# Performance work log

Measured on AMD Instinct MI355X. Metric: run time of the kernel, lower is better.

Reference implementation:

```python
import jax, jax.numpy as jnp
import numpy as np

FEAT = 128
N_RBF = 20
CUTOFF = 5.0
N_GRAPHS = 128
ATOMS = 64
N_ATOMS = N_GRAPHS * ATOMS  # 8192
N_EDGES = N_ATOMS * 32      # 262144


def setup_inputs() -> dict:
    key = jax.random.key(0)
    ks = jax.random.split(key, 12)
    s_j = jax.random.normal(ks[0], (N_ATOMS, FEAT), jnp.float32)
    v_j = jax.random.normal(ks[1], (N_ATOMS, FEAT, 3), jnp.float32)
    r_ij = jax.random.normal(ks[2], (N_EDGES, 3), jnp.float32) * 1.5
    nbrs = jax.random.randint(ks[3], (N_EDGES, 2), 0, N_ATOMS, dtype=jnp.int32)
    num_atoms = jnp.full((N_GRAPHS,), ATOMS, dtype=jnp.int32)
    sc = 0.05
    W1 = jax.random.normal(ks[4], (FEAT, FEAT), jnp.float32) * sc
    b1 = jnp.zeros((FEAT,), jnp.float32)
    W2 = jax.random.normal(ks[5], (FEAT, 3 * FEAT), jnp.float32) * sc
    b2 = jnp.zeros((3 * FEAT,), jnp.float32)
    Wr = jax.random.normal(ks[6], (N_RBF, 3 * FEAT), jnp.float32) * sc
    br = jnp.zeros((3 * FEAT,), jnp.float32)
    Wd = jax.random.normal(ks[7], (FEAT, 3 * FEAT), jnp.float32) * sc
    bd = jnp.zeros((3 * FEAT,), jnp.float32)
    return {"s_j": s_j, "v_j": v_j, "r_ij": r_ij, "nbrs": nbrs,
            "num_atoms": num_atoms, "W1": W1, "b1": b1, "W2": W2, "b2": b2,
            "Wr": Wr, "br": br, "Wd": Wd, "bd": bd}


def _forward(s_j, v_j, r_ij, nbrs, W1, b1, W2, b2, Wr, br, Wd, bd):
    # preprocess_r
    dist = jnp.linalg.norm(r_ij, axis=-1)            # [E]
    unit = r_ij / dist[:, None]                      # [E,3]

    # InvariantMessage: per-atom MLP, gather at nbrs[:,1], times radial filter
    phi = jax.nn.silu(s_j @ W1 + b1) @ W2 + b2       # [N, 3F]
    phi_e = phi[nbrs[:, 1]]                          # [E, 3F]
    n = jnp.arange(1, N_RBF + 1, dtype=jnp.float32)
    rbf = jnp.sin(n[None, :] * jnp.pi * dist[:, None] / CUTOFF) / dist[:, None]  # [E, n_rbf]
    env = jnp.where(dist < CUTOFF, 0.5 * (jnp.cos(jnp.pi * dist / CUTOFF) + 1.0), 0.0)
    w_s = (rbf @ Wr + br) * env[:, None]             # [E, 3F]
    inv_out = (phi_e * w_s).reshape(-1, 3, FEAT)     # [E, 3, F]

    split_0 = inv_out[:, 0, :][..., None]            # [E, F, 1]
    split_1 = inv_out[:, 1, :]                       # [E, F]
    split_2 = inv_out[:, 2, :][..., None]            # [E, F, 1]

    unit_add = split_2 * unit[:, None, :]            # [E, F, 3]
    delta_v_ij = unit_add + split_0 * v_j[nbrs[:, 1]]  # [E, F, 3]
    delta_s_ij = split_1                             # [E, F]

    seg = nbrs[:, 0]
    delta_v_i = jax.ops.segment_sum(delta_v_ij, seg, num_segments=N_ATOMS)
    delta_s_l = jax.ops.segment_sum(delta_s_ij, seg, num_segments=N_ATOMS)

    # NonLocalInteraction: per-graph exact softmax attention (uniform graph size)
    qkv = s_j @ Wd + bd                              # [N, 3F]
    Q, K, V = jnp.split(qkv, 3, axis=-1)
    Qb = Q.reshape(N_GRAPHS, ATOMS, FEAT)
    Kb = K.reshape(N_GRAPHS, ATOMS, FEAT)
    Vb = V.reshape(N_GRAPHS, ATOMS, FEAT)
    scores = jnp.einsum('bqf,bkf->bqk', Qb, Kb) / jnp.sqrt(jnp.float32(FEAT))
    att = jnp.einsum('bqk,bkf->bqf', jax.nn.softmax(scores, axis=-1), Vb)
    delta_s_nl = att.reshape(N_ATOMS, FEAT)

    delta_s_i = delta_s_l + delta_s_nl
    return delta_s_i, delta_v_i


def reference(s_j, v_j, r_ij, nbrs, num_atoms, W1, b1, W2, b2, Wr, br, Wd, bd):
    # num_atoms is uniform (ATOMS per graph); attention is batched accordingly.
    return _forward(s_j, v_j, r_ij, nbrs, W1, b1, W2, b2, Wr, br, Wd, bd)
```

## Files before the change

kernel.cpp:

```cpp
#include <hip/hip_runtime.h>
#include <hip/hip_bf16.h>
#include <cstdint>

#define FEAT    128
#define NRBF    20
#define NATOMS  8192
#define NEDGES  262144
#define NGRAPH  128
#define APG     64
#define PI_F    3.14159265358979323846f
#define CUTOFF_F 5.0f
#define TABUS   ((size_t)NATOMS * 64 * 6)

typedef unsigned int uint_t;
typedef unsigned short ushort_t;
typedef __attribute__((ext_vector_type(4))) float f32x4;
typedef __attribute__((ext_vector_type(4))) short short4v;
typedef __attribute__((ext_vector_type(8))) short short8;
struct U3 { uint_t x, y, z; };

__device__ __forceinline__ float bflo(uint_t u) { return __uint_as_float(u << 16); }
__device__ __forceinline__ float bfhi(uint_t u) { return __uint_as_float(u & 0xffff0000u); }
__device__ __forceinline__ float bfus(ushort_t u) { return __uint_as_float((uint_t)u << 16); }
__device__ __forceinline__ ushort_t f2bf(float f) {
  uint_t u = __float_as_uint(f);
  return (ushort_t)((u + 0x7fffu + ((u >> 16) & 1u)) >> 16);
}
__device__ __forceinline__ uint_t pack2(float lo, float hi) {
  return (uint_t)f2bf(lo) | ((uint_t)f2bf(hi) << 16);
}
__device__ __forceinline__ float pick4(float a0, float a1, float a2, float a3, int g) {
  return (g == 0) ? a0 : (g == 1) ? a1 : (g == 2) ? a2 : a3;
}

__device__ __forceinline__ ushort_t swz_elem(const float* __restrict__ W, int N,
                                             int NT, int i) {
  int jj = i & 7, lane = (i >> 3) & 63, tile = i >> 9;
  int ks = tile / NT, ctg = tile - ks * NT;
  int g = lane >> 4, q = lane & 15;
  int k = 32 * ks + 4 * g + (jj & 3) + 16 * (jj >> 2);
  int c = 16 * ctg + q;
  return f2bf(W[(size_t)k * N + c]);
}

__global__ void prep_kernel(const float* __restrict__ v_j, const float* __restrict__ W1,
                            const float* __restrict__ W2, const float* __restrict__ Wd,
                            const float* __restrict__ Wr, const float* __restrict__ br,
                            ushort_t* __restrict__ PV, ushort_t* __restrict__ w1s,
                            ushort_t* __restrict__ w2s, ushort_t* __restrict__ wds,
                            ushort_t* __restrict__ wrs) {
  int i = blockIdx.x * 256 + threadIdx.x;
  if (i < NATOMS * FEAT) {
    int j = i >> 7, f = i & 127;
    int h = f >> 6, fl = f & 63;
    const float* vp = v_j + (size_t)i * 3;
    ushort_t* rp = PV + (size_t)h * TABUS + ((size_t)j * 64 + fl) * 6;
    uint_t* o = reinterpret_cast<uint_t*>(rp);
    o[0] = 0u;
    o[1] = pack2(0.f, vp[0]);
    o[2] = pack2(vp[1], vp[2]);
    return;
  }
  i -= NATOMS * FEAT;
  if (i < 16384) { w1s[i] = swz_elem(W1, 128, 8, i); return; }
  i -= 16384;
  if (i < 49152) { w2s[i] = swz_elem(W2, 384, 24, i); return; }
  i -= 49152;
  if (i < 49152) { wds[i] = swz_elem(Wd, 384, 24, i); return; }
  i -= 49152;
  if (i < 12288) {
    int jj = i & 7, lane = (i >> 3) & 63, ct = i >> 9;
    int g = lane >> 4, q = lane & 15;
    int k = 4 * g + (jj & 3) + 16 * (jj >> 2);
    int f = 16 * ct + q;
    float v = (k < NRBF) ? Wr[k * 384 + f] : (k == NRBF ? br[f] : 0.f);
    wrs[i] = f2bf(v);
  }
}

__global__ __launch_bounds__(256) void gemm_mfma(
    const void* __restrict__ Asrc, int a_f32, const ushort_t* __restrict__ Wswz,
    const float* __restrict__ bias, int N, int NT, int silu, int omode,
    void* __restrict__ p0, void* __restrict__ p1) {
  __shared__ ushort_t As[64][136];
  const int t = threadIdx.x;
  const int r0 = blockIdx.x * 64, c0 = blockIdx.y * 64;
  const int w = t >> 6, l = t & 63, g = l >> 4, q = l & 15;

  short8 bf[4][4];
  #pragma unroll
  for (int ks = 0; ks < 4; ++ks)
    #pragma unroll
    for (int ct = 0; ct < 4; ++ct)
      bf[ks][ct] = *reinterpret_cast<const short8*>(
          Wswz + ((size_t)(ks * NT + (c0 >> 4) + ct) * 64 + l) * 8);

  if (a_f32) {
    const float* Af = (const float*)Asrc;
    for (int i = t; i < 64 * 32; i += 256) {
      int r = i >> 5, k4 = i & 31;
      float4 v = *reinterpret_cast<const float4*>(Af + (size_t)(r0 + r) * 128 + 4 * k4);
      ushort4 o = {f2bf(v.x), f2bf(v.y), f2bf(v.z), f2bf(v.w)};
      *reinterpret_cast<ushort4*>(&As[r][4 * k4]) = o;
    }
  } else {
    const ushort_t* Ab = (const ushort_t*)Asrc;
    for (int i = t; i < 64 * 16; i += 256) {
      int r = i >> 4, g8 = i & 15;
      short8 v = *reinterpret_cast<const short8*>(Ab + (size_t)(r0 + r) * 128 + 8 * g8);
      *reinterpret_cast<short8*>(&As[r][8 * g8]) = v;
    }
  }
  __syncthreads();

  f32x4 acc[4] = {};
  #pragma unroll
  for (int ks = 0; ks < 4; ++ks) {
    const ushort_t* ap = &As[16 * w + q][32 * ks + 4 * g];
    short4v alo = *reinterpret_cast<const short4v*>(ap);
    short4v ahi = *reinterpret_cast<const short4v*>(ap + 16);
    short8 af;
    af[0] = alo[0]; af[1] = alo[1]; af[2] = alo[2]; af[3] = alo[3];
    af[4] = ahi[0]; af[5] = ahi[1]; af[6] = ahi[2]; af[7] = ahi[3];
    #pragma unroll
    for (int ct = 0; ct < 4; ++ct)
      acc[ct] = __builtin_amdgcn_mfma_f32_16x16x32_bf16(af, bf[ks][ct], acc[ct], 0, 0, 0);
  }

  #pragma unroll
  for (int ct = 0; ct < 4; ++ct) {
    int col = c0 + 16 * ct + q;
    float bb = bias[col];
    #pragma unroll
    for (int r = 0; r < 4; ++r) {
      float o = acc[ct][r] + bb;
      if (silu) o = o / (1.f + __expf(-o));
      int row = r0 + 16 * w + 4 * g + r;
      if (omode == 1) {
        ((ushort_t*)p0)[(size_t)row * N + col] = f2bf(o);
      } else if (omode == 2) {
        int f = col & 127, s = col >> 7;
        int hh = f >> 6, fl = f & 63;
        ((ushort_t*)p0)[(size_t)hh * TABUS + ((size_t)row * 64 + fl) * 6 + s] = f2bf(o);
      } else {
        if (col < 128) ((float*)p0)[(size_t)row * 128 + col] = o;
        else           ((ushort_t*)p1)[(size_t)row * 256 + col - 128] = f2bf(o);
      }
    }
  }
}

__global__ void hist_kernel(const int* __restrict__ nbrs, int* __restrict__ counts) {
  int e = blockIdx.x * blockDim.x + threadIdx.x;
  if (e < NEDGES) atomicAdd(&counts[nbrs[2 * e]], 1);
}

__global__ __launch_bounds__(1024) void scan_kernel(
    const int* __restrict__ counts, int* __restrict__ offs, int* __restrict__ cursor) {
  __shared__ int part[1024];
  const int t = threadIdx.x;
  int local[8];
  int s = 0;
  #pragma unroll
  for (int i = 0; i < 8; ++i) { local[i] = counts[t * 8 + i]; s += local[i]; }
  part[t] = s;
  __syncthreads();
  for (int off = 1; off < 1024; off <<= 1) {
    int v = part[t];
    int add = (t >= off) ? part[t - off] : 0;
    __syncthreads();
    part[t] = v + add;
    __syncthreads();
  }
  int excl = part[t] - s;
  #pragma unroll
  for (int i = 0; i < 8; ++i) {
    offs[t * 8 + i] = excl;
    cursor[t * 8 + i] = excl;
    excl += local[i];
  }
  if (t == 1023) offs[NATOMS] = excl;
}

__global__ void scatter_kernel(const int* __restrict__ nbrs, int* __restrict__ cursor,
                               int* __restrict__ sorted) {
  int e = blockIdx.x * blockDim.x + threadIdx.x;
  if (e < NEDGES) {
    int seg = nbrs[2 * e];
    int pos = atomicAdd(&cursor[seg], 1);
    sorted[pos] = e;
  }
}

__global__ __launch_bounds__(256) void edge_mfma6(
    const int* __restrict__ sorted, const int* __restrict__ offs,
    const int* __restrict__ nbrs, const float* __restrict__ r_ij,
    const ushort_t* __restrict__ PV, const ushort_t* __restrict__ wrs,
    float* __restrict__ out_s, float* __restrict__ out_v) {
  __shared__ short8 sW[12 * 64];
  const int t = threadIdx.x;
  const int h = blockIdx.x & 1;
  for (int i = t; i < 12 * 64; i += 256) {
    int tl = i >> 6, l2 = i & 63;
    int s = tl >> 2, c = tl & 3;
    sW[i] = *reinterpret_cast<const short8*>(
        wrs + ((size_t)(s * 8 + 4 * h + c) * 64 + l2) * 8);
  }
  __syncthreads();

  const int w = t >> 6, l = t & 63, g = l >> 4, q = l & 15;
  const int atom = (blockIdx.x >> 1) * 4 + w;
  const int start = offs[atom], end = offs[atom + 1];
  const float c1 = PI_F / CUTOFF_F;
  const char* PVb = reinterpret_cast<const char*>(PV) + (size_t)h * TABUS * 2;

  float ds[4] = {};
  float dv[4][3] = {};

  for (int eb = start; eb < end; eb += 16) {
    float ang = 0.f, ie = 0.f, env = 0.f, u0 = 0.f, u1 = 0.f, u2 = 0.f;
    int jn = 0;
    if (eb + q < end) {
      int e = sorted[eb + q];
      float x = r_ij[3 * e], y = r_ij[3 * e + 1], z = r_ij[3 * e + 2];
      jn = nbrs[2 * e + 1];
      float d = sqrtf(x * x + y * y + z * z);
      float inv = 1.f / d;
      ang = c1 * d;
      env = (d < CUTOFF_F) ? 0.5f * (__cosf(ang) + 1.f) : 0.f;
      ie = inv * env;
      u0 = x * inv; u1 = y * inv; u2 = z * inv;
    }
    const char* pb[4];
    float ub[4][3];
    #pragma unroll
    for (int r = 0; r < 4; ++r) {
      int src = 4 * g + r;
      int jr = __shfl(jn, src, 64);
      ub[r][0] = __shfl(u0, src, 64);
      ub[r][1] = __shfl(u1, src, 64);
      ub[r][2] = __shfl(u2, src, 64);
      pb[r] = PVb + (size_t)jr * 768 + (size_t)q * 12;
    }
    U3 ld[4][4];
    #pragma unroll
    for (int c = 0; c < 4; ++c)
      #pragma unroll
      for (int r = 0; r < 4; ++r)
        ld[c][r] = *reinterpret_cast<const U3*>(pb[r] + (size_t)c * 192);
    short8 af;
    #pragma unroll
    for (int jj = 0; jj < 8; ++jj) {
      int k = 4 * g + (jj & 3) + 16 * (jj >> 2);
      float v = (k < NRBF) ? ie * __sinf((float)(k + 1) * ang)
                           : (k == NRBF ? env : 0.f);
      af[jj] = (short)f2bf(v);
    }
    #pragma unroll
    for (int c = 0; c < 4; ++c) {
      short8 b0 = sW[(0 * 4 + c) * 64 + l];
      short8 b1 = sW[(1 * 4 + c) * 64 + l];
      short8 b2 = sW[(2 * 4 + c) * 64 + l];
      f32x4 z4 = {0.f, 0.f, 0.f, 0.f};
      f32x4 cs0 = __builtin_amdgcn_mfma_f32_16x16x32_bf16(af, b0, z4, 0, 0, 0);
      f32x4 cs1 = __builtin_amdgcn_mfma_f32_16x16x32_bf16(af, b1, z4, 0, 0, 0);
      f32x4 cs2 = __builtin_amdgcn_mfma_f32_16x16x32_bf16(af, b2, z4, 0, 0, 0);
      #pragma unroll
      for (int r = 0; r < 4; ++r) {
        U3 u = ld[c][r];
        float p0 = bflo(u.x), p1 = bfhi(u.x);
        float p2 = bflo(u.y), v0 = bfhi(u.y);
        float v1 = bflo(u.z), v2 = bfhi(u.z);
        float pw0 = p0 * cs0[r];
        ds[c] += p1 * cs1[r];
        float pw2 = p2 * cs2[r];
        dv[c][0] += pw0 * v0 + pw2 * ub[r][0];
        dv[c][1] += pw0 * v1 + pw2 * ub[r][1];
        dv[c][2] += pw0 * v2 + pw2 * ub[r][2];
      }
    }
  }

  #pragma unroll
  for (int c = 0; c < 4; ++c) {
    float x = ds[c];
    x += __shfl_xor(x, 16, 64); x += __shfl_xor(x, 32, 64);
    ds[c] = x;
    #pragma unroll
    for (int cc = 0; cc < 3; ++cc) {
      float y = dv[c][cc];
      y += __shfl_xor(y, 16, 64); y += __shfl_xor(y, 32, 64);
      dv[c][cc] = y;
    }
  }
  float sv = pick4(ds[0], ds[1], ds[2], ds[3], g);
  float d0 = pick4(dv[0][0], dv[1][0], dv[2][0], dv[3][0], g);
  float d1 = pick4(dv[0][1], dv[1][1], dv[2][1], dv[3][1], g);
  float d2 = pick4(dv[0][2], dv[1][2], dv[2][2], dv[3][2], g);
  int f = 64 * h + 16 * g + q;
  out_s[(size_t)atom * FEAT + f] = sv;
  float* ov = out_v + (size_t)atom * 384 + (size_t)f * 3;
  ov[0] = d0; ov[1] = d1; ov[2] = d2;
}

__device__ __forceinline__ float wave_max64(float v) {
  #pragma unroll
  for (int m = 32; m > 0; m >>= 1) v = fmaxf(v, __shfl_xor(v, m, 64));
  return v;
}
__device__ __forceinline__ float wave_sum64(float v) {
  #pragma unroll
  for (int m = 32; m > 0; m >>= 1) v += __shfl_xor(v, m, 64);
  return v;
}

__global__ __launch_bounds__(256) void attn_kernel(const float* __restrict__ Qf,
                                                   const ushort_t* __restrict__ kvbf,
                                                   float* __restrict__ out_s) {
  __shared__ float4 Ks4[64 * 32];
  __shared__ float  Vs[64][130];
  __shared__ float  Ps[4][4][64];
  const int b = blockIdx.x >> 1, half = blockIdx.x & 1;
  const int t = threadIdx.x;
  const float* qbase = Qf + (size_t)b * APG * 128;
  const ushort_t* kvb = kvbf + (size_t)b * APG * 256;

  for (int i = t; i < 64 * 32; i += 256) {
    int a = i >> 5, gg = i & 31;
    ushort4 k4 = *reinterpret_cast<const ushort4*>(kvb + a * 256 + 4 * gg);
    float4 kf = {bfus(k4.x), bfus(k4.y), bfus(k4.z), bfus(k4.w)};
    Ks4[a * 32 + (gg ^ (a & 7))] = kf;
  }
  for (int i = t; i < 64 * 32; i += 256) {
    int a = i >> 5, gg = i & 31;
    ushort4 v4 = *reinterpret_cast<const ushort4*>(kvb + a * 256 + 128 + 4 * gg);
    Vs[a][4 * gg + 0] = bfus(v4.x); Vs[a][4 * gg + 1] = bfus(v4.y);
    Vs[a][4 * gg + 2] = bfus(v4.z); Vs[a][4 * gg + 3] = bfus(v4.w);
  }
  __syncthreads();

  const int w = t >> 6, l = t & 63;
  const float scale = 0.08838834764831845f;

  for (int qq = 8 * half + w; qq < 8 * half + 8; qq += 4) {
    const float* q0p = qbase + (size_t)(4 * qq + 0) * 128;
    const float* q1p = qbase + (size_t)(4 * qq + 1) * 128;
    const float* q2p = qbase + (size_t)(4 * qq + 2) * 128;
    const float* q3p = qbase + (size_t)(4 * qq + 3) * 128;
    float s0 = 0.f, s1 = 0.f, s2 = 0.f, s3 = 0.f;
    #pragma unroll 8
    for (int i = 0; i < 32; ++i) {
      float4 k = Ks4[l * 32 + (i ^ (l & 7))];
      float4 q0 = *reinterpret_cast<const float4*>(q0p + 4 * i);
      float4 q1 = *reinterpret_cast<const float4*>(q1p + 4 * i);
      float4 q2 = *reinterpret_cast<const float4*>(q2p + 4 * i);
      float4 q3 = *reinterpret_cast<const float4*>(q3p + 4 * i);
      s0 += q0.x * k.x + q0.y * k.y + q0.z * k.z + q0.w * k.w;
      s1 += q1.x * k.x + q1.y * k.y + q1.z * k.z + q1.w * k.w;
      s2 += q2.x * k.x + q2.y * k.y + q2.z * k.z + q2.w * k.w;
      s3 += q3.x * k.x + q3.y * k.y + q3.z * k.z + q3.w * k.w;
    }
    s0 *= scale; s1 *= scale; s2 *= scale; s3 *= scale;

    float p0 = __expf(s0 - wave_max64(s0));
    float p1 = __expf(s1 - wave_max64(s1));
    float p2 = __expf(s2 - wave_max64(s2));
    float p3 = __expf(s3 - wave_max64(s3));
    p0 /= wave_sum64(p0); p1 /= wave_sum64(p1);
    p2 /= wave_sum64(p2); p3 /= wave_sum64(p3);

    Ps[w][0][l] = p0; Ps[w][1][l] = p1; Ps[w][2][l] = p2; Ps[w][3][l] = p3;
    __threadfence_block();

    float a00 = 0.f, a01 = 0.f, a10 = 0.f, a11 = 0.f;
    float a20 = 0.f, a21 = 0.f, a30 = 0.f, a31 = 0.f;
    for (int a = 0; a < 64; ++a) {
      float2 v = *reinterpret_cast<const float2*>(&Vs[a][2 * l]);
      float pa0 = Ps[w][0][a], pa1 = Ps[w][1][a];
      float pa2 = Ps[w][2][a], pa3 = Ps[w][3][a];
      a00 += pa0 * v.x; a01 += pa0 * v.y;
      a10 += pa1 * v.x; a11 += pa1 * v.y;
      a20 += pa2 * v.x; a21 += pa2 * v.y;
      a30 += pa3 * v.x; a31 += pa3 * v.y;
    }
    size_t row0 = (size_t)(b * APG + 4 * qq) * FEAT + 2 * l;
    float2* o0 = reinterpret_cast<float2*>(out_s + row0);
    float2* o1 = reinterpret_cast<float2*>(out_s + row0 + FEAT);
    float2* o2 = reinterpret_cast<float2*>(out_s + row0 + 2 * FEAT);
    float2* o3 = reinterpret_cast<float2*>(out_s + row0 + 3 * FEAT);
    float2 c0 = *o0; c0.x += a00; c0.y += a01; *o0 = c0;
    float2 c1 = *o1; c1.x += a10; c1.y += a11; *o1 = c1;
    float2 c2 = *o2; c2.x += a20; c2.y += a21; *o2 = c2;
    float2 c3 = *o3; c3.x += a30; c3.y += a31; *o3 = c3;
    __threadfence_block();
  }
}

extern "C" void kernel_launch(void* const* d_in, const int* in_sizes, int n_in,
                              void* d_out, int out_size, void* d_ws, size_t ws_size,
                              hipStream_t stream) {
  const float* s_j  = (const float*)d_in[0];
  const float* v_j  = (const float*)d_in[1];
  const float* r_ij = (const float*)d_in[2];
  const int*   nbrs = (const int*)d_in[3];
  const float* W1   = (const float*)d_in[5];
  const float* b1   = (const float*)d_in[6];
  const float* W2   = (const float*)d_in[7];
  const float* b2   = (const float*)d_in[8];
  const float* Wr   = (const float*)d_in[9];
  const float* br   = (const float*)d_in[10];
  const float* Wd   = (const float*)d_in[11];
  const float* bd   = (const float*)d_in[12];

  float* out_s = (float*)d_out;
  float* out_v = out_s + (size_t)NATOMS * FEAT;

  float*    Qf   = (float*)d_ws;
  ushort_t* kvbf = (ushort_t*)(Qf + NATOMS * FEAT);
  ushort_t* PV   = kvbf + (size_t)NATOMS * 256;
  ushort_t* w1s  = PV + 2 * TABUS;
  ushort_t* w2s  = w1s + 16384;
  ushort_t* wds  = w2s + 49152;
  ushort_t* wrs  = wds + 49152;
  ushort_t* h_bf = wrs + 12288;
  int* sorted = (int*)h_bf;
  int* offs   = sorted + NEDGES;
  int* cursor = offs + (NATOMS + 1);
  int* counts = cursor + NATOMS;

  int prep_total = NATOMS * FEAT + 16384 + 49152 + 49152 + 12288;
  prep_kernel<<<(prep_total + 255) / 256, 256, 0, stream>>>(
      v_j, W1, W2, Wd, Wr, br, PV, w1s, w2s, wds, wrs);

  gemm_mfma<<<dim3(NATOMS / 64, 2), 256, 0, stream>>>(
      s_j, 1, w1s, b1, 128, 8, 1, 1, h_bf, nullptr);
  gemm_mfma<<<dim3(NATOMS / 64, 6), 256, 0, stream>>>(
      h_bf, 0, w2s, b2, 384, 24, 0, 2, PV, nullptr);

  hipMemsetAsync(counts, 0, NATOMS * sizeof(int), stream);
  hist_kernel<<<NEDGES / 256, 256, 0, stream>>>(nbrs, counts);
  scan_kernel<<<1, 1024, 0, stream>>>(counts, offs, cursor);
  scatter_kernel<<<NEDGES / 256, 256, 0, stream>>>(nbrs, cursor, sorted);

  gemm_mfma<<<dim3(NATOMS / 64, 6), 256, 0, stream>>>(
      s_j, 1, wds, bd, 384, 24, 0, 3, Qf, kvbf);

  edge_mfma6<<<NATOMS / 2, 256, 0, stream>>>(sorted, offs, nbrs, r_ij, PV,
                                             wrs, out_s, out_v);
  attn_kernel<<<NGRAPH * 2, 256, 0, stream>>>(Qf, kvbf, out_s);
}
```

Baseline: 161.4 us.

## Pack sorted edge records and split edge kernel into feature quarters

The scatter kernel now writes a packed per-edge record (neighbour index plus r vector) in segment-sorted order, so the edge kernel reads one contiguous 16-byte load instead of an index followed by dependent gathers. The edge kernel also prefetches the next chunk's record. The PV table and radial weights are re-laid out into four 32-feature quarters, doubling the grid and halving per-wave accumulators and loads. In exchange, the per-edge radial basis and A-fragment work is recomputed four times per atom instead of twice, and the scatter writes more bytes.

After: 146.6 us. -9.2%, faster.

```diff
diff --git a/kernel.cpp b/kernel.cpp
--- a/kernel.cpp
+++ b/kernel.cpp
@@ -10,7 +10,7 @@
 #define APG     64
 #define PI_F    3.14159265358979323846f
 #define CUTOFF_F 5.0f
-#define TABUS   ((size_t)NATOMS * 64 * 6)
+#define QTUS    ((size_t)NATOMS * 32 * 6)
 
 typedef unsigned int uint_t;
 typedef unsigned short ushort_t;
@@ -28,9 +28,6 @@
 }
 __device__ __forceinline__ uint_t pack2(float lo, float hi) {
   return (uint_t)f2bf(lo) | ((uint_t)f2bf(hi) << 16);
-}
-__device__ __forceinline__ float pick4(float a0, float a1, float a2, float a3, int g) {
-  return (g == 0) ? a0 : (g == 1) ? a1 : (g == 2) ? a2 : a3;
 }
 
 __device__ __forceinline__ ushort_t swz_elem(const float* __restrict__ W, int N,
@@ -52,10 +49,9 @@
   int i = blockIdx.x * 256 + threadIdx.x;
   if (i < NATOMS * FEAT) {
     int j = i >> 7, f = i & 127;
-    int h = f >> 6, fl = f & 63;
+    int tbl = f >> 5, fl = f & 31;
     const float* vp = v_j + (size_t)i * 3;
-    ushort_t* rp = PV + (size_t)h * TABUS + ((size_t)j * 64 + fl) * 6;
-    uint_t* o = reinterpret_cast<uint_t*>(rp);
+    uint_t* o = reinterpret_cast<uint_t*>(PV + (size_t)tbl * QTUS + ((size_t)j * 32 + fl) * 6);
     o[0] = 0u;
     o[1] = pack2(0.f, vp[0]);
     o[2] = pack2(vp[1], vp[2]);
@@ -140,8 +136,8 @@
         ((ushort_t*)p0)[(size_t)row * N + col] = f2bf(o);
       } else if (omode == 2) {
         int f = col & 127, s = col >> 7;
-        int hh = f >> 6, fl = f & 63;
-        ((ushort_t*)p0)[(size_t)hh * TABUS + ((size_t)row * 64 + fl) * 6 + s] = f2bf(o);
+        int tbl = f >> 5, fl = f & 31;
+        ((ushort_t*)p0)[(size_t)tbl * QTUS + ((size_t)row * 32 + fl) * 6 + s] = f2bf(o);
       } else {
         if (col < 128) ((float*)p0)[(size_t)row * 128 + col] = o;
         else           ((ushort_t*)p1)[(size_t)row * 256 + col - 128] = f2bf(o);
@@ -182,48 +178,53 @@
   if (t == 1023) offs[NATOMS] = excl;
 }
 
-__global__ void scatter_kernel(const int* __restrict__ nbrs, int* __restrict__ cursor,
-                               int* __restrict__ sorted) {
+__global__ void scatter_kernel(const int* __restrict__ nbrs, const float* __restrict__ r_ij,
+                               int* __restrict__ cursor, uint4* __restrict__ erec) {
   int e = blockIdx.x * blockDim.x + threadIdx.x;
   if (e < NEDGES) {
-    int seg = nbrs[2 * e];
-    int pos = atomicAdd(&cursor[seg], 1);
-    sorted[pos] = e;
-  }
-}
-
-__global__ __launch_bounds__(256) void edge_mfma6(
-    const int* __restrict__ sorted, const int* __restrict__ offs,
-    const int* __restrict__ nbrs, const float* __restrict__ r_ij,
+    int2 nb = *reinterpret_cast<const int2*>(nbrs + 2 * e);
+    int pos = atomicAdd(&cursor[nb.x], 1);
+    const float* rp = r_ij + 3 * e;
+    erec[pos] = make_uint4((uint_t)nb.y, __float_as_uint(rp[0]),
+                           __float_as_uint(rp[1]), __float_as_uint(rp[2]));
+  }
+}
+
+__global__ __launch_bounds__(256) void edge_mfma7(
+    const uint4* __restrict__ erec, const int* __restrict__ offs,
     const ushort_t* __restrict__ PV, const ushort_t* __restrict__ wrs,
     float* __restrict__ out_s, float* __restrict__ out_v) {
-  __shared__ short8 sW[12 * 64];
+  __shared__ short8 sW[6 * 64];
   const int t = threadIdx.x;
-  const int h = blockIdx.x & 1;
-  for (int i = t; i < 12 * 64; i += 256) {
+  const int qtr = blockIdx.x & 3;
+  for (int i = t; i < 6 * 64; i += 256) {
     int tl = i >> 6, l2 = i & 63;
-    int s = tl >> 2, c = tl & 3;
+    int s = tl >> 1, c = tl & 1;
     sW[i] = *reinterpret_cast<const short8*>(
-        wrs + ((size_t)(s * 8 + 4 * h + c) * 64 + l2) * 8);
+        wrs + ((size_t)(s * 8 + 2 * qtr + c) * 64 + l2) * 8);
   }
   __syncthreads();
 
   const int w = t >> 6, l = t & 63, g = l >> 4, q = l & 15;
-  const int atom = (blockIdx.x >> 1) * 4 + w;
+  const int atom = (blockIdx.x >> 2) * 4 + w;
   const int start = offs[atom], end = offs[atom + 1];
   const float c1 = PI_F / CUTOFF_F;
-  const char* PVb = reinterpret_cast<const char*>(PV) + (size_t)h * TABUS * 2;
-
-  float ds[4] = {};
-  float dv[4][3] = {};
+  const char* PVb = reinterpret_cast<const char*>(PV) + (size_t)qtr * QTUS * 2;
+
+  float ds[2] = {};
+  float dv[2][3] = {};
+
+  uint4 er = make_uint4(0u, 0u, 0u, 0u);
+  if (start + q < end) er = erec[start + q];
 
   for (int eb = start; eb < end; eb += 16) {
+    uint4 ern = make_uint4(0u, 0u, 0u, 0u);
+    if (eb + 16 + q < end) ern = erec[eb + 16 + q];
     float ang = 0.f, ie = 0.f, env = 0.f, u0 = 0.f, u1 = 0.f, u2 = 0.f;
     int jn = 0;
     if (eb + q < end) {
-      int e = sorted[eb + q];
-      float x = r_ij[3 * e], y = r_ij[3 * e + 1], z = r_ij[3 * e + 2];
-      jn = nbrs[2 * e + 1];
+      jn = (int)er.x;
+      float x = __uint_as_float(er.y), y = __uint_as_float(er.z), z = __uint_as_float(er.w);
       float d = sqrtf(x * x + y * y + z * z);
       float inv = 1.f / d;
       ang = c1 * d;
@@ -240,11 +241,11 @@
       ub[r][0] = __shfl(u0, src, 64);
       ub[r][1] = __shfl(u1, src, 64);
       ub[r][2] = __shfl(u2, src, 64);
-      pb[r] = PVb + (size_t)jr * 768 + (size_t)q * 12;
-    }
-    U3 ld[4][4];
-    #pragma unroll
-    for (int c = 0; c < 4; ++c)
+      pb[r] = PVb + (size_t)jr * 384 + (size_t)q * 12;
+    }
+    U3 ld[2][4];
+    #pragma unroll
+    for (int c = 0; c < 2; ++c)
       #pragma unroll
       for (int r = 0; r < 4; ++r)
         ld[c][r] = *reinterpret_cast<const U3*>(pb[r] + (size_t)c * 192);
@@ -257,10 +258,10 @@
       af[jj] = (short)f2bf(v);
     }
     #pragma unroll
-    for (int c = 0; c < 4; ++c) {
-      short8 b0 = sW[(0 * 4 + c) * 64 + l];
-      short8 b1 = sW[(1 * 4 + c) * 64 + l];
-      short8 b2 = sW[(2 * 4 + c) * 64 + l];
+    for (int c = 0; c < 2; ++c) {
+      short8 b0 = sW[(0 * 2 + c) * 64 + l];
+      short8 b1 = sW[(1 * 2 + c) * 64 + l];
+      short8 b2 = sW[(2 * 2 + c) * 64 + l];
       f32x4 z4 = {0.f, 0.f, 0.f, 0.f};
       f32x4 cs0 = __builtin_amdgcn_mfma_f32_16x16x32_bf16(af, b0, z4, 0, 0, 0);
       f32x4 cs1 = __builtin_amdgcn_mfma_f32_16x16x32_bf16(af, b1, z4, 0, 0, 0);
@@ -279,10 +280,11 @@
         dv[c][2] += pw0 * v2 + pw2 * ub[r][2];
       }
     }
-  }
-
-  #pragma unroll
-  for (int c = 0; c < 4; ++c) {
+    er = ern;
+  }
+
+  #pragma unroll
+  for (int c = 0; c < 2; ++c) {
     float x = ds[c];
     x += __shfl_xor(x, 16, 64); x += __shfl_xor(x, 32, 64);
     ds[c] = x;
@@ -293,14 +295,16 @@
       dv[c][cc] = y;
     }
   }
-  float sv = pick4(ds[0], ds[1], ds[2], ds[3], g);
-  float d0 = pick4(dv[0][0], dv[1][0], dv[2][0], dv[3][0], g);
-  float d1 = pick4(dv[0][1], dv[1][1], dv[2][1], dv[3][1], g);
-  float d2 = pick4(dv[0][2], dv[1][2], dv[2][2], dv[3][2], g);
-  int f = 64 * h + 16 * g + q;
-  out_s[(size_t)atom * FEAT + f] = sv;
-  float* ov = out_v + (size_t)atom * 384 + (size_t)f * 3;
-  ov[0] = d0; ov[1] = d1; ov[2] = d2;
+  if (g < 2) {
+    float sv = (g == 0) ? ds[0] : ds[1];
+    float d0 = (g == 0) ? dv[0][0] : dv[1][0];
+    float d1 = (g == 0) ? dv[0][1] : dv[1][1];
+    float d2 = (g == 0) ? dv[0][2] : dv[1][2];
+    int f = 32 * qtr + 16 * g + q;
+    out_s[(size_t)atom * FEAT + f] = sv;
+    float* ov = out_v + (size_t)atom * 384 + (size_t)f * 3;
+    ov[0] = d0; ov[1] = d1; ov[2] = d2;
+  }
 }
 
 __device__ __forceinline__ float wave_max64(float v) {
@@ -418,13 +422,13 @@
   float*    Qf   = (float*)d_ws;
   ushort_t* kvbf = (ushort_t*)(Qf + NATOMS * FEAT);
   ushort_t* PV   = kvbf + (size_t)NATOMS * 256;
-  ushort_t* w1s  = PV + 2 * TABUS;
+  ushort_t* w1s  = PV + 4 * QTUS;
   ushort_t* w2s  = w1s + 16384;
   ushort_t* wds  = w2s + 49152;
   ushort_t* wrs  = wds + 49152;
   ushort_t* h_bf = wrs + 12288;
-  int* sorted = (int*)h_bf;
-  int* offs   = sorted + NEDGES;
+  uint4*    erec = (uint4*)h_bf;
+  int* offs   = (int*)((char*)h_bf + 4194304);
   int* cursor = offs + (NATOMS + 1);
   int* counts = cursor + NATOMS;
 
@@ -440,12 +444,11 @@
   hipMemsetAsync(counts, 0, NATOMS * sizeof(int), stream);
   hist_kernel<<<NEDGES / 256, 256, 0, stream>>>(nbrs, counts);
   scan_kernel<<<1, 1024, 0, stream>>>(counts, offs, cursor);
-  scatter_kernel<<<NEDGES / 256, 256, 0, stream>>>(nbrs, cursor, sorted);
+  scatter_kernel<<<NEDGES / 256, 256, 0, stream>>>(nbrs, r_ij, cursor, erec);
 
   gemm_mfma<<<dim3(NATOMS / 64, 6), 256, 0, stream>>>(
       s_j, 1, wds, bd, 384, 24, 0, 3, Qf, kvbf);
 
-  edge_mfma6<<<NATOMS / 2, 256, 0, stream>>>(sorted, offs, nbrs, r_ij, PV,
-                                             wrs, out_s, out_v);
+  edge_mfma7<<<NATOMS, 256, 0, stream>>>(erec, offs, PV, wrs, out_s, out_v);
   attn_kernel<<<NGRAPH * 2, 256, 0, stream>>>(Qf, kvbf, out_s);
 }
```
